# Performance work log

Hardware: AMD Instinct MI355X
Metric: run time of the kernel (lower is better)

Reference implementation:

```python
import jax, jax.numpy as jnp
import numpy as np

EPS = 1e-6  # F.normalize eps

N, C, H, W = 2, 64, 64, 64
HEADS, DK, DV = 2, 64, 32


def setup_inputs() -> dict:
    key = jax.random.key(0)
    ks = jax.random.split(key, 9)
    w = lambda k, sh: jax.random.normal(k, sh, jnp.float32) * 0.05
    return {
        "x":  jax.random.normal(ks[0], (N, C, H, W), jnp.float32),
        "Wq": w(ks[1], (HEADS, DK, C)), "bq": w(ks[2], (HEADS, DK)),
        "Wk": w(ks[3], (HEADS, DK, C)), "bk": w(ks[4], (HEADS, DK)),
        "Wv": w(ks[5], (HEADS, DV, C)), "bv": w(ks[6], (HEADS, DV)),
        "Wm": w(ks[7], (C, HEADS * DV)), "bm": w(ks[8], (C,)),
    }


def _l2norm(t):
    # F.normalize(dim=1) on [N, dk, L]; here heads are stacked: [N, h, dk, L], axis=2
    n = jnp.linalg.norm(t, axis=2, keepdims=True)
    return t / jnp.maximum(n, EPS)


def reference(x, Wq, bq, Wk, bk, Wv, bv, Wm, bm):
    n, c, h, w = x.shape
    L = h * w
    xf = x.reshape(n, c, L)  # 1x1 conv == pointwise channel GEMM; x_enc = x (no pos enc)
    Q = jnp.einsum('hkc,ncl->nhkl', Wq, xf) + bq[None, :, :, None]
    K = jnp.einsum('hkc,ncl->nhkl', Wk, xf) + bk[None, :, :, None]
    V = jnp.einsum('hvc,ncl->nhvl', Wv, xf) + bv[None, :, :, None]
    Q = _l2norm(Q)
    K = _l2norm(K)
    # cosine-similarity attention: contract over dk, softmax over keys
    A = jax.nn.softmax(jnp.einsum('nhkl,nhkm->nhlm', Q, K), axis=-1)  # [n,h,L,L]
    R = jnp.einsum('nhlm,nhvm->nhvl', A, V)  # [n,h,dv,L]
    Rc = R.reshape(n, -1, L)  # concat heads along channels
    out = jnp.einsum('oc,ncl->nol', Wm, Rc) + bm[None, :, None]
    return out.reshape(n, c, h, w) + x  # residual
```

## Files before the change

kernel.cpp:

```cpp
#include <hip/hip_runtime.h>
#include <cmath>


typedef __bf16 bf16x8 __attribute__((ext_vector_type(8)));
typedef __bf16 bf16x4 __attribute__((ext_vector_type(4)));
typedef float f4_t __attribute__((ext_vector_type(4)));

#define LQ 4096
#define NH 4
#define KS 8

__device__ inline f4_t mfma16(bf16x8 a, bf16x8 b, f4_t c) {
    return __builtin_amdgcn_mfma_f32_16x16x32_bf16(a, b, c, 0, 0, 0);
}

__global__ void k0_prep(const float* __restrict__ Wq, const float* __restrict__ bq,
                        const float* __restrict__ Wk, const float* __restrict__ bk,
                        const float* __restrict__ Wv, const float* __restrict__ bv,
                        __bf16* __restrict__ Wb, float* __restrict__ bb) {
    const int tid = threadIdx.x;
    const int row = blockIdx.x * 64 + (tid >> 2);
    const int c0  = (tid & 3) * 16;

    const float* wsrc;
    float bval;
    if (row < 128)      { wsrc = Wq + (size_t)row * 64;         bval = bq[row]; }
    else if (row < 256) { wsrc = Wk + (size_t)(row - 128) * 64; bval = bk[row - 128]; }
    else                { wsrc = Wv + (size_t)(row - 256) * 64; bval = bv[row - 256]; }

#pragma unroll
    for (int j = 0; j < 16; ++j)
        Wb[(size_t)row * 64 + c0 + j] = (__bf16)wsrc[c0 + j];
    if ((tid & 3) == 0) bb[row] = bval;
}

__global__ __launch_bounds__(256) void k1_qkv(
        const float* __restrict__ x,
        const __bf16* __restrict__ Wb, const float* __restrict__ bb,
        __bf16* __restrict__ Qb, __bf16* __restrict__ Kb,
        __bf16* __restrict__ Vtb) {
    const int tid  = threadIdx.x;
    const int lane = tid & 63;
    const int w    = tid >> 6;
    const int quad = lane >> 4;
    const int l15  = lane & 15;
    const int lt   = blockIdx.x;
    const int n    = blockIdx.y;
    const int l0   = lt * 32;

    __shared__ __bf16 xl[32][72];

    {
        const int c0 = tid >> 5, l = tid & 31;
#pragma unroll
        for (int i = 0; i < 8; ++i) {
            const int c = c0 + i * 8;
            xl[l][c] = (__bf16)x[((size_t)n * 64 + c) * LQ + l0 + l];
        }
    }

    bf16x8 af[4][2], av[2];
#pragma unroll
    for (int t = 0; t < 4; ++t)
#pragma unroll
        for (int kh = 0; kh < 2; ++kh)
            af[t][kh] = *(const bf16x8*)(Wb +
                (size_t)(w * 64 + t * 16 + l15) * 64 + kh * 32 + quad * 8);
#pragma unroll
    for (int kh = 0; kh < 2; ++kh)
        av[kh] = *(const bf16x8*)(Wb +
            (size_t)(256 + w * 16 + l15) * 64 + kh * 32 + quad * 8);

    f4_t binit[4], bvinit;
#pragma unroll
    for (int t = 0; t < 4; ++t)
#pragma unroll
        for (int r = 0; r < 4; ++r)
            binit[t][r] = bb[w * 64 + t * 16 + quad * 4 + r];
#pragma unroll
    for (int r = 0; r < 4; ++r)
        bvinit[r] = bb[256 + w * 16 + quad * 4 + r];

    __syncthreads();

    f4_t acc[4][2], vacc[2];
#pragma unroll
    for (int lsub = 0; lsub < 2; ++lsub) {
        bf16x8 bf0 = *(const bf16x8*)&xl[lsub * 16 + l15][quad * 8];
        bf16x8 bf1 = *(const bf16x8*)&xl[lsub * 16 + l15][32 + quad * 8];
#pragma unroll
        for (int t = 0; t < 4; ++t) {
            f4_t a = mfma16(af[t][0], bf0, binit[t]);
            acc[t][lsub] = mfma16(af[t][1], bf1, a);
        }
        f4_t va = mfma16(av[0], bf0, bvinit);
        vacc[lsub] = mfma16(av[1], bf1, va);
    }

    const int nh = n * 2 + (w & 1);
    __bf16* dst  = (w < 2) ? Qb : Kb;
#pragma unroll
    for (int lsub = 0; lsub < 2; ++lsub) {
        float ss = 0.f;
#pragma unroll
        for (int t = 0; t < 4; ++t)
#pragma unroll
            for (int r = 0; r < 4; ++r)
                ss = fmaf(acc[t][lsub][r], acc[t][lsub][r], ss);
        ss += __shfl_xor(ss, 16, 64);
        ss += __shfl_xor(ss, 32, 64);
        const float rn = 1.0f / fmaxf(sqrtf(ss), 1e-6f);

        const int l = l0 + lsub * 16 + l15;
#pragma unroll
        for (int t = 0; t < 4; ++t) {
            bf16x4 pk;
#pragma unroll
            for (int r = 0; r < 4; ++r) pk[r] = (__bf16)(acc[t][lsub][r] * rn);
            const int kc = t * 2 + (quad >> 1);
            *(bf16x4*)(dst + ((size_t)(nh * 8 + kc) * LQ + l) * 8 + (quad & 1) * 4) = pk;
        }
#pragma unroll
        for (int r = 0; r < 4; ++r) {
            const int vrow = w * 16 + quad * 4 + r;
            Vtb[(size_t)(n * 64 + vrow) * LQ + l] = (__bf16)vacc[lsub][r];
        }
    }
}

__global__ __launch_bounds__(256, 4) void k2_attn(
        const __bf16* __restrict__ Qb, const __bf16* __restrict__ Kb,
        const __bf16* __restrict__ Vtb,
        float* __restrict__ numP, float* __restrict__ denP) {
    const int lane = threadIdx.x & 63;
    const int wave = threadIdx.x >> 6;
    const int quad = lane >> 4;
    const int l15  = lane & 15;
    const int nh   = blockIdx.y;
    const int ks   = blockIdx.z;
    const int qbase = blockIdx.x * 128 + wave * 32;
    const int kbase = ks * 512;

    __shared__ __bf16 P[4][2][16][40];

    const f4_t fzero = {0.f, 0.f, 0.f, 0.f};

    bf16x8 qf[2][2];
#pragma unroll
    for (int qt = 0; qt < 2; ++qt)
#pragma unroll
        for (int kh = 0; kh < 2; ++kh)
            qf[qt][kh] = *(const bf16x8*)(Qb +
                ((size_t)(nh * 8 + kh * 4 + quad) * LQ + qbase + qt * 16 + l15) * 8);

    f4_t racc[2][2];
#pragma unroll
    for (int a = 0; a < 2; ++a)
#pragma unroll
        for (int b = 0; b < 2; ++b) racc[a][b] = fzero;
    float den[2] = {0.f, 0.f};

    for (int ch = 0; ch < 16; ++ch) {
        const int kb = kbase + ch * 32;

        bf16x8 kf[2][2], vf[2];
#pragma unroll
        for (int kt = 0; kt < 2; ++kt)
#pragma unroll
            for (int kh = 0; kh < 2; ++kh)
                kf[kt][kh] = *(const bf16x8*)(Kb +
                    ((size_t)(nh * 8 + kh * 4 + quad) * LQ + kb + kt * 16 + l15) * 8);
#pragma unroll
        for (int vt = 0; vt < 2; ++vt)
            vf[vt] = *(const bf16x8*)(Vtb +
                (size_t)(nh * 32 + vt * 16 + l15) * LQ + kb + quad * 8);

#pragma unroll
        for (int qt = 0; qt < 2; ++qt) {
#pragma unroll
            for (int kt = 0; kt < 2; ++kt) {
                f4_t s = mfma16(kf[kt][0], qf[qt][0], fzero);
                s      = mfma16(kf[kt][1], qf[qt][1], s);
                bf16x4 pv;
                float d = 0.f;
#pragma unroll
                for (int r = 0; r < 4; ++r) {
                    float p = __expf(s[r]);
                    d += p;
                    pv[r] = (__bf16)p;
                }
                den[qt] += d;
                *(bf16x4*)&P[wave][qt][l15][kt * 16 + quad * 4] = pv;
            }
            bf16x8 pf = *(const bf16x8*)&P[wave][qt][l15][quad * 8];
#pragma unroll
            for (int vt = 0; vt < 2; ++vt)
                racc[vt][qt] = mfma16(vf[vt], pf, racc[vt][qt]);
        }
    }

#pragma unroll
    for (int qt = 0; qt < 2; ++qt) {
        den[qt] += __shfl_xor(den[qt], 16, 64);
        den[qt] += __shfl_xor(den[qt], 32, 64);
    }

    const size_t pb = (size_t)(nh * KS + ks) * LQ;
#pragma unroll
    for (int vt = 0; vt < 2; ++vt)
#pragma unroll
        for (int qt = 0; qt < 2; ++qt)
#pragma unroll
            for (int r = 0; r < 4; ++r)
                numP[(pb + qbase + qt * 16 + l15) * 32 + vt * 16 + quad * 4 + r]
                    = racc[vt][qt][r];

    if (lane < 16)
#pragma unroll
        for (int qt = 0; qt < 2; ++qt)
            denP[pb + qbase + qt * 16 + lane] = den[qt];
}

__global__ __launch_bounds__(256) void k3_out(
        const float* __restrict__ numP, const float* __restrict__ denP,
        const float* __restrict__ Wm, const float* __restrict__ bm,
        const float* __restrict__ x, float* __restrict__ out) {
    const int tid  = threadIdx.x;
    const int lane = tid & 63;
    const int wv   = tid >> 6;
    const int n    = blockIdx.x >> 6;
    const int lt   = blockIdx.x & 63;
    const int l0   = lt * 64;

    __shared__ float Rf[64][65];
    __shared__ float dinv[2][64];

    if (tid < 128) {
        const int hh = tid >> 6, li = tid & 63;
        float s = 0.f;
#pragma unroll
        for (int k = 0; k < KS; ++k)
            s += denP[(size_t)((n * 2 + hh) * KS + k) * LQ + l0 + li];
        dinv[hh][li] = 1.0f / s;
    }

    {
        const int v = tid & 31, lsub = tid >> 5;
#pragma unroll
        for (int hh = 0; hh < 2; ++hh) {
            const size_t base = (size_t)(n * 2 + hh) * KS * LQ;
#pragma unroll
            for (int i = 0; i < 8; ++i) {
                const int l = lsub + 8 * i;
                float s = 0.f;
#pragma unroll
                for (int k = 0; k < KS; ++k)
                    s += numP[(base + (size_t)k * LQ + l0 + l) * 32 + v];
                Rf[hh * 32 + v][l] = s;
            }
        }
    }
    __syncthreads();

    const float d0 = dinv[0][lane], d1 = dinv[1][lane];
    float rj[64];
#pragma unroll
    for (int j = 0; j < 64; ++j)
        rj[j] = Rf[j][lane] * (j < 32 ? d0 : d1);

    float acc[16];
#pragma unroll
    for (int oi = 0; oi < 16; ++oi) acc[oi] = bm[wv * 16 + oi];
#pragma unroll
    for (int oi = 0; oi < 16; ++oi) {
        const float* wr = Wm + (size_t)(wv * 16 + oi) * 64;
        float a = acc[oi];
#pragma unroll
        for (int j4 = 0; j4 < 16; ++j4) {
            f4_t t = *(const f4_t*)(wr + j4 * 4);
            a = fmaf(t[0], rj[j4 * 4 + 0], a);
            a = fmaf(t[1], rj[j4 * 4 + 1], a);
            a = fmaf(t[2], rj[j4 * 4 + 2], a);
            a = fmaf(t[3], rj[j4 * 4 + 3], a);
        }
        acc[oi] = a;
    }

#pragma unroll
    for (int oi = 0; oi < 16; ++oi) {
        const int o = wv * 16 + oi;
        const size_t idx = (size_t)(n * 64 + o) * LQ + l0 + lane;
        out[idx] = acc[oi] + x[idx];
    }
}

extern "C" void kernel_launch(void* const* d_in, const int* in_sizes, int n_in,
                              void* d_out, int out_size, void* d_ws, size_t ws_size,
                              hipStream_t stream) {
    const float* x  = (const float*)d_in[0];
    const float* Wq = (const float*)d_in[1];
    const float* bq = (const float*)d_in[2];
    const float* Wk = (const float*)d_in[3];
    const float* bk = (const float*)d_in[4];
    const float* Wv = (const float*)d_in[5];
    const float* bv = (const float*)d_in[6];
    const float* Wm = (const float*)d_in[7];
    const float* bm = (const float*)d_in[8];
    float* out = (float*)d_out;

    __bf16* Qb  = (__bf16*)d_ws;
    __bf16* Kb  = Qb + (size_t)NH * LQ * 64;
    __bf16* Vtb = Kb + (size_t)NH * LQ * 64;
    float*  numP = (float*)(Vtb + (size_t)NH * 32 * LQ);
    float*  denP = numP + (size_t)NH * KS * 32 * LQ;
    __bf16* Wb  = (__bf16*)(denP + (size_t)NH * KS * LQ);
    float*  bb  = (float*)(Wb + 320 * 64);

    k0_prep<<<dim3(5), dim3(256), 0, stream>>>(Wq, bq, Wk, bk, Wv, bv, Wb, bb);
    k1_qkv<<<dim3(128, 2), dim3(256), 0, stream>>>(x, Wb, bb, Qb, Kb, Vtb);
    k2_attn<<<dim3(32, NH, KS), dim3(256), 0, stream>>>(Qb, Kb, Vtb, numP, denP);
    k3_out<<<dim3(128), dim3(256), 0, stream>>>(numP, denP, Wm, bm, x, out);
}
```

Measured before the change: 124.9 us.

## Stage K tiles in double-buffered LDS shared across waves in attention kernel

The four waves of a block used to load the same K chunk from global memory on their own. Each chunk is now fetched once per block into a double-buffered shared-memory tile, with the next chunk prefetched while the current one is used. The QK MFMAs, exp/softmax and PV stages are also split into separate batched phases to expose more instruction-level parallelism. In exchange it adds a block-wide barrier every chunk, extra LDS traffic, and more live registers for the batched score tiles.

Result: faster. 120.6 us (-3.4%).

```diff
diff --git a/kernel.cpp b/kernel.cpp
--- a/kernel.cpp
+++ b/kernel.cpp
@@ -132,8 +132,9 @@
         const __bf16* __restrict__ Qb, const __bf16* __restrict__ Kb,
         const __bf16* __restrict__ Vtb,
         float* __restrict__ numP, float* __restrict__ denP) {
-    const int lane = threadIdx.x & 63;
-    const int wave = threadIdx.x >> 6;
+    const int tid  = threadIdx.x;
+    const int lane = tid & 63;
+    const int wave = tid >> 6;
     const int quad = lane >> 4;
     const int l15  = lane & 15;
     const int nh   = blockIdx.y;
@@ -141,9 +142,14 @@
     const int qbase = blockIdx.x * 128 + wave * 32;
     const int kbase = ks * 512;
 
+    __shared__ __bf16 Kl[2][2048];
     __shared__ __bf16 P[4][2][16][40];
 
     const f4_t fzero = {0.f, 0.f, 0.f, 0.f};
+
+    const int s_kc = ((tid >> 6) & 1) * 4 + ((tid >> 4) & 3);
+    const int s_l  = ((tid >> 7) << 4) | (tid & 15);
+    const __bf16* s_src = Kb + ((size_t)(nh * 8 + s_kc) * LQ + kbase + s_l) * 8;
 
     bf16x8 qf[2][2];
 #pragma unroll
@@ -160,43 +166,66 @@
         for (int b = 0; b < 2; ++b) racc[a][b] = fzero;
     float den[2] = {0.f, 0.f};
 
+    *(bf16x8*)&Kl[0][tid * 8] = *(const bf16x8*)s_src;
+    __syncthreads();
+
     for (int ch = 0; ch < 16; ++ch) {
+        const int cur = ch & 1;
+
+        if (ch < 15)
+            *(bf16x8*)&Kl[cur ^ 1][tid * 8] =
+                *(const bf16x8*)(s_src + (size_t)(ch + 1) * 32 * 8);
+
         const int kb = kbase + ch * 32;
 
-        bf16x8 kf[2][2], vf[2];
-#pragma unroll
-        for (int kt = 0; kt < 2; ++kt)
-#pragma unroll
-            for (int kh = 0; kh < 2; ++kh)
-                kf[kt][kh] = *(const bf16x8*)(Kb +
-                    ((size_t)(nh * 8 + kh * 4 + quad) * LQ + kb + kt * 16 + l15) * 8);
+        bf16x8 vf[2];
 #pragma unroll
         for (int vt = 0; vt < 2; ++vt)
             vf[vt] = *(const bf16x8*)(Vtb +
                 (size_t)(nh * 32 + vt * 16 + l15) * LQ + kb + quad * 8);
 
-#pragma unroll
-        for (int qt = 0; qt < 2; ++qt) {
+        bf16x8 kf[2][2];
+#pragma unroll
+        for (int kt = 0; kt < 2; ++kt)
+#pragma unroll
+            for (int kh = 0; kh < 2; ++kh)
+                kf[kt][kh] = *(const bf16x8*)
+                    &Kl[cur][(kt * 128 + kh * 64 + quad * 16 + l15) * 8];
+
+        f4_t s[2][2];
+#pragma unroll
+        for (int qt = 0; qt < 2; ++qt)
 #pragma unroll
             for (int kt = 0; kt < 2; ++kt) {
-                f4_t s = mfma16(kf[kt][0], qf[qt][0], fzero);
-                s      = mfma16(kf[kt][1], qf[qt][1], s);
+                f4_t t = mfma16(kf[kt][0], qf[qt][0], fzero);
+                s[qt][kt] = mfma16(kf[kt][1], qf[qt][1], t);
+            }
+
+#pragma unroll
+        for (int qt = 0; qt < 2; ++qt)
+#pragma unroll
+            for (int kt = 0; kt < 2; ++kt) {
                 bf16x4 pv;
                 float d = 0.f;
 #pragma unroll
                 for (int r = 0; r < 4; ++r) {
-                    float p = __expf(s[r]);
+                    float p = __expf(s[qt][kt][r]);
                     d += p;
                     pv[r] = (__bf16)p;
                 }
                 den[qt] += d;
                 *(bf16x4*)&P[wave][qt][l15][kt * 16 + quad * 4] = pv;
             }
+
+#pragma unroll
+        for (int qt = 0; qt < 2; ++qt) {
             bf16x8 pf = *(const bf16x8*)&P[wave][qt][l15][quad * 8];
 #pragma unroll
             for (int vt = 0; vt < 2; ++vt)
                 racc[vt][qt] = mfma16(vf[vt], pf, racc[vt][qt]);
         }
+
+        __syncthreads();
     }
 
 #pragma unroll
```
